# Performance work log

Hardware: AMD Instinct MI355X
Metric: run time of the kernel (lower is better)

The kernel has to match this reference:

```python
import jax, jax.numpy as jnp
import numpy as np

NUM_HEADS = 8
KEY_SIZE = 64
VALUE_SIZE = 64
NUM_GROUPS = 3 * NUM_HEADS  # 24
C = NUM_HEADS * (2 * KEY_SIZE + VALUE_SIZE)  # 1536
EPS = 1e-5


def setup_inputs() -> dict:
    key = jax.random.key(0)
    k1, k2, k3 = jax.random.split(key, 3)
    x = jax.random.normal(k1, (8, C, 32, 32), dtype=jnp.float32)
    # GroupNorm affine params (torch default ones/zeros, perturbed for non-trivial grads)
    gn_weight = 1.0 + 0.1 * jax.random.normal(k2, (C,), dtype=jnp.float32)
    gn_bias = 0.1 * jax.random.normal(k3, (C,), dtype=jnp.float32)
    return {"x": x, "gn_weight": gn_weight, "gn_bias": gn_bias}


def _group_norm(x, weight, bias):
    B, Cc, H, W = x.shape
    xg = x.reshape(B, NUM_GROUPS, -1)  # [B, G, (C/G)*H*W]
    mean = jnp.mean(xg, axis=-1, keepdims=True)
    var = jnp.var(xg, axis=-1, keepdims=True)
    xn = ((xg - mean) * jax.lax.rsqrt(var + EPS)).reshape(B, Cc, H, W)
    return xn * weight[:, None, None] + bias[:, None, None]


def reference(x, gn_weight, gn_bias):
    NH, KS, VS = NUM_HEADS, KEY_SIZE, VALUE_SIZE
    B, Cc, H, W = x.shape
    xn = _group_norm(x, gn_weight, gn_bias)
    xr = xn.reshape(B, NH, 2 * KS + VS, H * W)  # [B, NH, 2KS+VS, NK]
    k = xr[:, :, :KS]            # [B, NH, KS, NK]
    q = xr[:, :, KS:2 * KS]      # [B, NH, KS, NK]
    v = xr[:, :, 2 * KS:]        # [B, NH, VS, NK]
    # saliency = q^T @ k / sqrt(KS) -> [B, NH, NKq, NKk]
    sal = jnp.einsum('bhcq,bhck->bhqk', q, k) / jnp.sqrt(jnp.float32(KS))
    mask = jax.nn.softmax(sal, axis=-1)
    # out = v @ mask^T -> [B, NH, VS, NKq]
    out = jnp.einsum('bhvk,bhqk->bhvq', v, mask)
    return out.reshape(B, NH * VS, H, W)
```

## Files before the change

### kernel.cpp

```cpp
#include <hip/hip_runtime.h>
#include <hip/hip_bf16.h>


typedef __attribute__((ext_vector_type(8))) short bf16x8;
typedef __attribute__((ext_vector_type(4))) float f32x4;
typedef __attribute__((ext_vector_type(16))) float f32x16;
typedef unsigned short u16;
typedef unsigned int u32;

#define SM_SCALE 0.18033688f
#define SM_OFF   8.0f

__device__ __forceinline__ u32 pack2(float a, float b) {
    union { float f; u32 u; } ua, ub; ua.f = a; ub.f = b;
    return __builtin_amdgcn_perm(ub.u + 0x8000u, ua.u + 0x8000u, 0x07060302u);
}
union BB { uint4 u; bf16x8 v; };

__device__ __forceinline__ f32x16 zero16() {
    f32x16 z;
#pragma unroll
    for (int i = 0; i < 16; ++i) z[i] = 0.f;
    return z;
}

__device__ __forceinline__ void swap32(u32 a, u32 b, int hi, u32& ret0, u32& ret1) {
#if __has_builtin(__builtin_amdgcn_permlane32_swap)
    (void)hi;
    auto sw = __builtin_amdgcn_permlane32_swap(a, b, false, false);
    ret0 = sw[0]; ret1 = sw[1];
#else
    u32 pa = __shfl_xor(a, 32), pb = __shfl_xor(b, 32);
    ret0 = hi ? pb : a;
    ret1 = hi ? b : pa;
#endif
}

__global__ __launch_bounds__(256) void gn_partial(const float* __restrict__ x,
                                                  float* __restrict__ partials) {
    int blk = blockIdx.x;
    const float4* p = (const float4*)(x + (size_t)blk * 8192);
    int t = threadIdx.x;
    float s1a = 0.f, s2a = 0.f, s1b = 0.f, s2b = 0.f;
#pragma unroll
    for (int i = 0; i < 8; i += 2) {
        float4 va = p[t + i * 256];
        float4 vb = p[t + (i + 1) * 256];
        s1a += va.x + va.y + va.z + va.w;
        s2a += va.x*va.x + va.y*va.y + va.z*va.z + va.w*va.w;
        s1b += vb.x + vb.y + vb.z + vb.w;
        s2b += vb.x*vb.x + vb.y*vb.y + vb.z*vb.z + vb.w*vb.w;
    }
    float s1 = s1a + s1b, s2 = s2a + s2b;
    for (int off = 32; off > 0; off >>= 1) {
        s1 += __shfl_down(s1, off);
        s2 += __shfl_down(s2, off);
    }
    __shared__ float a1[4], a2[4];
    int wave = t >> 6, lane = t & 63;
    if (lane == 0) { a1[wave] = s1; a2[wave] = s2; }
    __syncthreads();
    if (t == 0) {
        partials[blk * 2 + 0] = a1[0] + a1[1] + a1[2] + a1[3];
        partials[blk * 2 + 1] = a2[0] + a2[1] + a2[2] + a2[3];
    }
}

__device__ __forceinline__ void group_stats(const float* __restrict__ partials,
                                            int bg, float& mean, float& rstd) {
    float s1 = 0.f, s2 = 0.f;
#pragma unroll
    for (int j = 0; j < 8; ++j) {
        s1 += partials[(bg * 8 + j) * 2 + 0];
        s2 += partials[(bg * 8 + j) * 2 + 1];
    }
    mean = s1 * (1.f / 65536.f);
    float var = s2 * (1.f / 65536.f) - mean * mean;
    rstd = rsqrtf(var + 1e-5f);
}

__global__ __launch_bounds__(256, 2) void attn_fused(
    const float* __restrict__ x, const float* __restrict__ gamma,
    const float* __restrict__ beta, const float* __restrict__ partials,
    float* __restrict__ out)
{
    const int bid = blockIdx.x;
    const int qt = bid >> 6;
    const int pair = bid & 63;
    const int b = pair >> 3, h = pair & 7;
    const float* xb = x + (size_t)b * 1536 * 1024;
    const int tid = threadIdx.x;
    const int w = tid >> 6;
    const int lane = tid & 63;
    const int li = lane & 31;
    const int hi = lane >> 5;

    float ms[3], rs[3];
    group_stats(partials, b * 24 + 3 * h + 0, ms[0], rs[0]);
    group_stats(partials, b * 24 + 3 * h + 1, ms[1], rs[1]);
    group_stats(partials, b * 24 + 3 * h + 2, ms[2], rs[2]);

    __shared__ uint4 KT[2][512];
    __shared__ uint4 VT[2][512];

    const int sr = tid & 63;
    const int cc0 = tid >> 6;
    float kw[16], kb[16];
#pragma unroll
    for (int u = 0; u < 16; ++u) {
        int c = ((u < 8) ? cc0 : (cc0 + 4)) * 8 + (u & 7);
        int cg = h * 192 + c;
        kw[u] = gamma[cg] * rs[0];
        kb[u] = beta[cg] - ms[0] * kw[u];
    }
    const int vcg = h * 192 + 128 + sr;
    const float vw = gamma[vcg] * rs[2];
    const float vb = beta[vcg] - ms[2] * vw;

    const int kx = sr & 7;
    const int kidx0 = sr * 8 + (cc0 ^ kx);
    const int kidx1 = sr * 8 + ((cc0 + 4) ^ kx);
    const int vidx0 = sr * 8 + ((cc0 * 2) ^ kx);
    const int vidx1 = sr * 8 + ((cc0 * 2 + 1) ^ kx);

    const float* kbase = xb + (size_t)(h * 192) * 1024 + sr;
    const float* vbase = xb + (size_t)vcg * 1024 + cc0 * 16;

    const int q0 = qt * 128 + w * 32;
    bf16x8 bq[4];
#pragma unroll
    for (int cs = 0; cs < 4; ++cs) {
        u32 qq[4];
#pragma unroll
        for (int jp = 0; jp < 4; ++jp) {
            int cg = h * 192 + 64 + cs * 16 + hi * 8 + jp * 2;
            float w0 = gamma[cg] * rs[1],     b0 = beta[cg] - ms[1] * w0;
            float w1 = gamma[cg + 1] * rs[1], b1 = beta[cg + 1] - ms[1] * w1;
            float a0 = xb[(size_t)cg * 1024 + q0 + li];
            float a1 = xb[(size_t)(cg + 1) * 1024 + q0 + li];
            qq[jp] = pack2(__builtin_fmaf(a0, w0, b0), __builtin_fmaf(a1, w1, b1));
        }
        BB tb; tb.u = uint4{qq[0], qq[1], qq[2], qq[3]};
        bq[cs] = tb.v;
    }

    f32x16 oacc[2];
    oacc[0] = zero16(); oacc[1] = zero16();
    float lsum = 0.f;

    const int x7 = li & 7;

    float rk[16], rv[16];
#define LOAD_TILE(KT_)                                                        \
    {                                                                         \
        const float* kp = kbase + (KT_) * 64;                                 \
        _Pragma("unroll")                                                     \
        for (int u = 0; u < 16; ++u) {                                        \
            int c = ((u < 8) ? cc0 : (cc0 + 4)) * 8 + (u & 7);                \
            rk[u] = kp[(size_t)c * 1024];                                     \
        }                                                                     \
        const float* vp = vbase + (KT_) * 64;                                 \
        _Pragma("unroll")                                                     \
        for (int f = 0; f < 4; ++f) {                                         \
            float4 vq = *(const float4*)(vp + f * 4);                         \
            rv[f * 4 + 0] = vq.x; rv[f * 4 + 1] = vq.y;                       \
            rv[f * 4 + 2] = vq.z; rv[f * 4 + 3] = vq.w;                       \
        }                                                                     \
    }
#define COMMIT_TILE(BUF_)                                                     \
    {                                                                         \
        uint4 ka, kc, va, vc;                                                 \
        ka.x = pack2(__builtin_fmaf(rk[0], kw[0], kb[0]),                     \
                     __builtin_fmaf(rk[1], kw[1], kb[1]));                    \
        ka.y = pack2(__builtin_fmaf(rk[2], kw[2], kb[2]),                     \
                     __builtin_fmaf(rk[3], kw[3], kb[3]));                    \
        ka.z = pack2(__builtin_fmaf(rk[4], kw[4], kb[4]),                     \
                     __builtin_fmaf(rk[5], kw[5], kb[5]));                    \
        ka.w = pack2(__builtin_fmaf(rk[6], kw[6], kb[6]),                     \
                     __builtin_fmaf(rk[7], kw[7], kb[7]));                    \
        kc.x = pack2(__builtin_fmaf(rk[8], kw[8], kb[8]),                     \
                     __builtin_fmaf(rk[9], kw[9], kb[9]));                    \
        kc.y = pack2(__builtin_fmaf(rk[10], kw[10], kb[10]),                  \
                     __builtin_fmaf(rk[11], kw[11], kb[11]));                 \
        kc.z = pack2(__builtin_fmaf(rk[12], kw[12], kb[12]),                  \
                     __builtin_fmaf(rk[13], kw[13], kb[13]));                 \
        kc.w = pack2(__builtin_fmaf(rk[14], kw[14], kb[14]),                  \
                     __builtin_fmaf(rk[15], kw[15], kb[15]));                 \
        va.x = pack2(__builtin_fmaf(rv[0], vw, vb),                           \
                     __builtin_fmaf(rv[1], vw, vb));                          \
        va.y = pack2(__builtin_fmaf(rv[2], vw, vb),                           \
                     __builtin_fmaf(rv[3], vw, vb));                          \
        va.z = pack2(__builtin_fmaf(rv[4], vw, vb),                           \
                     __builtin_fmaf(rv[5], vw, vb));                          \
        va.w = pack2(__builtin_fmaf(rv[6], vw, vb),                           \
                     __builtin_fmaf(rv[7], vw, vb));                          \
        vc.x = pack2(__builtin_fmaf(rv[8], vw, vb),                           \
                     __builtin_fmaf(rv[9], vw, vb));                          \
        vc.y = pack2(__builtin_fmaf(rv[10], vw, vb),                          \
                     __builtin_fmaf(rv[11], vw, vb));                         \
        vc.z = pack2(__builtin_fmaf(rv[12], vw, vb),                          \
                     __builtin_fmaf(rv[13], vw, vb));                         \
        vc.w = pack2(__builtin_fmaf(rv[14], vw, vb),                          \
                     __builtin_fmaf(rv[15], vw, vb));                         \
        KT[BUF_][kidx0] = ka; KT[BUF_][kidx1] = kc;                           \
        VT[BUF_][vidx0] = va; VT[BUF_][vidx1] = vc;                           \
    }

    LOAD_TILE(0);
    COMMIT_TILE(0);
    __syncthreads();

#pragma unroll 2
    for (int kt = 0; kt < 16; ++kt) {
        const int cur = kt & 1;
        if (kt < 15) LOAD_TILE(kt + 1);

        f32x16 sf[2];
#pragma unroll
        for (int kf = 0; kf < 2; ++kf) {
            bf16x8 ak[4];
#pragma unroll
            for (int cs = 0; cs < 4; ++cs)
                ak[cs] = ((const BB*)&KT[cur][(kf * 32 + li) * 8 + ((cs * 2 + hi) ^ x7)])->v;
            f32x16 acc = zero16();
            __builtin_amdgcn_s_setprio(1);
#pragma unroll
            for (int cs = 0; cs < 4; ++cs)
                acc = __builtin_amdgcn_mfma_f32_32x32x16_bf16(ak[cs], bq[cs], acc, 0, 0, 0);
            __builtin_amdgcn_s_setprio(0);
            sf[kf] = acc;
        }

        BB pbv[4];
#pragma unroll
        for (int kf = 0; kf < 2; ++kf)
#pragma unroll
            for (int s = 0; s < 2; ++s) {
                float p0 = exp2f(__builtin_fmaf(sf[kf][8 * s + 0], SM_SCALE, -SM_OFF));
                float p1 = exp2f(__builtin_fmaf(sf[kf][8 * s + 1], SM_SCALE, -SM_OFF));
                float p2 = exp2f(__builtin_fmaf(sf[kf][8 * s + 2], SM_SCALE, -SM_OFF));
                float p3 = exp2f(__builtin_fmaf(sf[kf][8 * s + 3], SM_SCALE, -SM_OFF));
                float p4 = exp2f(__builtin_fmaf(sf[kf][8 * s + 4], SM_SCALE, -SM_OFF));
                float p5 = exp2f(__builtin_fmaf(sf[kf][8 * s + 5], SM_SCALE, -SM_OFF));
                float p6 = exp2f(__builtin_fmaf(sf[kf][8 * s + 6], SM_SCALE, -SM_OFF));
                float p7 = exp2f(__builtin_fmaf(sf[kf][8 * s + 7], SM_SCALE, -SM_OFF));
                lsum += ((p0 + p1) + (p2 + p3)) + ((p4 + p5) + (p6 + p7));
                u32 Pa = pack2(p0, p1), Pb = pack2(p2, p3);
                u32 Pc = pack2(p4, p5), Pd = pack2(p6, p7);
                u32 w0, w1, w2, w3;
                swap32(Pa, Pc, hi, w0, w2);
                swap32(Pb, Pd, hi, w1, w3);
                pbv[kf * 2 + s].u = uint4{w0, w1, w2, w3};
            }

#pragma unroll
        for (int vf = 0; vf < 2; ++vf) {
            bf16x8 av[4];
#pragma unroll
            for (int ks = 0; ks < 4; ++ks)
                av[ks] = ((const BB*)&VT[cur][(vf * 32 + li) * 8 + ((ks * 2 + hi) ^ x7)])->v;
            __builtin_amdgcn_s_setprio(1);
#pragma unroll
            for (int ks = 0; ks < 4; ++ks)
                oacc[vf] = __builtin_amdgcn_mfma_f32_32x32x16_bf16(av[ks], pbv[ks].v, oacc[vf], 0, 0, 0);
            __builtin_amdgcn_s_setprio(0);
        }

        if (kt < 15) COMMIT_TILE(cur ^ 1);
        __syncthreads();
    }

    lsum += __shfl_xor(lsum, 32);
    float invl = 1.f / lsum;
    float* ob = out + (size_t)pair * 65536 + q0 + li;
#pragma unroll
    for (int vf = 0; vf < 2; ++vf)
#pragma unroll
        for (int r = 0; r < 16; ++r) {
            int v = vf * 32 + (r & 3) + 8 * (r >> 2) + 4 * hi;
            ob[(size_t)v * 1024] = oacc[vf][r] * invl;
        }
}

extern "C" void kernel_launch(void* const* d_in, const int* in_sizes, int n_in,
                              void* d_out, int out_size, void* d_ws, size_t ws_size,
                              hipStream_t stream) {
    const float* x     = (const float*)d_in[0];
    const float* gamma = (const float*)d_in[1];
    const float* beta  = (const float*)d_in[2];
    float* out = (float*)d_out;

    float* partials = (float*)d_ws;

    gn_partial<<<1536, 256, 0, stream>>>(x, partials);
    attn_fused<<<512, 256, 0, stream>>>(x, gamma, beta, partials, out);
}
```

Measured before the change: 129.6 us.

## Split key sequence across two warp groups per block with LDS reduction

Doubles the block to 512 threads. Two 256-thread groups each process half of the key tiles (8 of 16) for the same query tile, each with its own double-buffered LDS tiles. Partial output accumulators and row sums are then combined through shared memory before the final normalised store. The goal is to halve the serial key loop per block and raise wave-level parallelism per CU. The cost is higher register and LDS pressure under the tighter launch bounds, duplicated Q loading, and an extra reduction step. The score MFMA and exp stages are also interleaved per key fragment, which cuts the live score registers.

```diff
diff --git a/kernel.cpp b/kernel.cpp
--- a/kernel.cpp
+++ b/kernel.cpp
@@ -79,7 +79,7 @@
     rstd = rsqrtf(var + 1e-5f);
 }
 
-__global__ __launch_bounds__(256, 2) void attn_fused(
+__global__ __launch_bounds__(512, 4) void attn_fused(
     const float* __restrict__ x, const float* __restrict__ gamma,
     const float* __restrict__ beta, const float* __restrict__ partials,
     float* __restrict__ out)
@@ -90,8 +90,10 @@
     const int b = pair >> 3, h = pair & 7;
     const float* xb = x + (size_t)b * 1536 * 1024;
     const int tid = threadIdx.x;
-    const int w = tid >> 6;
-    const int lane = tid & 63;
+    const int wg = tid >> 8;
+    const int t = tid & 255;
+    const int w2 = t >> 6;
+    const int lane = t & 63;
     const int li = lane & 31;
     const int hi = lane >> 5;
 
@@ -100,11 +102,10 @@
     group_stats(partials, b * 24 + 3 * h + 1, ms[1], rs[1]);
     group_stats(partials, b * 24 + 3 * h + 2, ms[2], rs[2]);
 
-    __shared__ uint4 KT[2][512];
-    __shared__ uint4 VT[2][512];
-
-    const int sr = tid & 63;
-    const int cc0 = tid >> 6;
+    __shared__ uint4 TILES[2][2][2][512];
+
+    const int sr = t & 63;
+    const int cc0 = t >> 6;
     float kw[16], kb[16];
 #pragma unroll
     for (int u = 0; u < 16; ++u) {
@@ -126,7 +127,7 @@
     const float* kbase = xb + (size_t)(h * 192) * 1024 + sr;
     const float* vbase = xb + (size_t)vcg * 1024 + cc0 * 16;
 
-    const int q0 = qt * 128 + w * 32;
+    const int q0 = qt * 128 + w2 * 32;
     bf16x8 bq[4];
 #pragma unroll
     for (int cs = 0; cs < 4; ++cs) {
@@ -151,15 +152,15 @@
     const int x7 = li & 7;
 
     float rk[16], rv[16];
-#define LOAD_TILE(KT_)                                                        \
+#define LOAD_TILE(KTG_)                                                       \
     {                                                                         \
-        const float* kp = kbase + (KT_) * 64;                                 \
+        const float* kp = kbase + (KTG_) * 64;                                \
         _Pragma("unroll")                                                     \
         for (int u = 0; u < 16; ++u) {                                        \
             int c = ((u < 8) ? cc0 : (cc0 + 4)) * 8 + (u & 7);                \
             rk[u] = kp[(size_t)c * 1024];                                     \
         }                                                                     \
-        const float* vp = vbase + (KT_) * 64;                                 \
+        const float* vp = vbase + (KTG_) * 64;                                \
         _Pragma("unroll")                                                     \
         for (int f = 0; f < 4; ++f) {                                         \
             float4 vq = *(const float4*)(vp + f * 4);                         \
@@ -202,63 +203,58 @@
                      __builtin_fmaf(rv[13], vw, vb));                         \
         vc.w = pack2(__builtin_fmaf(rv[14], vw, vb),                          \
                      __builtin_fmaf(rv[15], vw, vb));                         \
-        KT[BUF_][kidx0] = ka; KT[BUF_][kidx1] = kc;                           \
-        VT[BUF_][vidx0] = va; VT[BUF_][vidx1] = vc;                           \
-    }
-
-    LOAD_TILE(0);
+        TILES[wg][BUF_][0][kidx0] = ka; TILES[wg][BUF_][0][kidx1] = kc;       \
+        TILES[wg][BUF_][1][vidx0] = va; TILES[wg][BUF_][1][vidx1] = vc;       \
+    }
+
+    LOAD_TILE(wg * 8);
     COMMIT_TILE(0);
     __syncthreads();
 
 #pragma unroll 2
-    for (int kt = 0; kt < 16; ++kt) {
-        const int cur = kt & 1;
-        if (kt < 15) LOAD_TILE(kt + 1);
-
-        f32x16 sf[2];
+    for (int kt8 = 0; kt8 < 8; ++kt8) {
+        const int cur = kt8 & 1;
+        if (kt8 < 7) LOAD_TILE(wg * 8 + kt8 + 1);
+
+        BB pbv[4];
 #pragma unroll
         for (int kf = 0; kf < 2; ++kf) {
             bf16x8 ak[4];
 #pragma unroll
             for (int cs = 0; cs < 4; ++cs)
-                ak[cs] = ((const BB*)&KT[cur][(kf * 32 + li) * 8 + ((cs * 2 + hi) ^ x7)])->v;
+                ak[cs] = ((const BB*)&TILES[wg][cur][0][(kf * 32 + li) * 8 + ((cs * 2 + hi) ^ x7)])->v;
             f32x16 acc = zero16();
             __builtin_amdgcn_s_setprio(1);
 #pragma unroll
             for (int cs = 0; cs < 4; ++cs)
                 acc = __builtin_amdgcn_mfma_f32_32x32x16_bf16(ak[cs], bq[cs], acc, 0, 0, 0);
             __builtin_amdgcn_s_setprio(0);
-            sf[kf] = acc;
-        }
-
-        BB pbv[4];
-#pragma unroll
-        for (int kf = 0; kf < 2; ++kf)
 #pragma unroll
             for (int s = 0; s < 2; ++s) {
-                float p0 = exp2f(__builtin_fmaf(sf[kf][8 * s + 0], SM_SCALE, -SM_OFF));
-                float p1 = exp2f(__builtin_fmaf(sf[kf][8 * s + 1], SM_SCALE, -SM_OFF));
-                float p2 = exp2f(__builtin_fmaf(sf[kf][8 * s + 2], SM_SCALE, -SM_OFF));
-                float p3 = exp2f(__builtin_fmaf(sf[kf][8 * s + 3], SM_SCALE, -SM_OFF));
-                float p4 = exp2f(__builtin_fmaf(sf[kf][8 * s + 4], SM_SCALE, -SM_OFF));
-                float p5 = exp2f(__builtin_fmaf(sf[kf][8 * s + 5], SM_SCALE, -SM_OFF));
-                float p6 = exp2f(__builtin_fmaf(sf[kf][8 * s + 6], SM_SCALE, -SM_OFF));
-                float p7 = exp2f(__builtin_fmaf(sf[kf][8 * s + 7], SM_SCALE, -SM_OFF));
+                float p0 = exp2f(__builtin_fmaf(acc[8 * s + 0], SM_SCALE, -SM_OFF));
+                float p1 = exp2f(__builtin_fmaf(acc[8 * s + 1], SM_SCALE, -SM_OFF));
+                float p2 = exp2f(__builtin_fmaf(acc[8 * s + 2], SM_SCALE, -SM_OFF));
+                float p3 = exp2f(__builtin_fmaf(acc[8 * s + 3], SM_SCALE, -SM_OFF));
+                float p4 = exp2f(__builtin_fmaf(acc[8 * s + 4], SM_SCALE, -SM_OFF));
+                float p5 = exp2f(__builtin_fmaf(acc[8 * s + 5], SM_SCALE, -SM_OFF));
+                float p6 = exp2f(__builtin_fmaf(acc[8 * s + 6], SM_SCALE, -SM_OFF));
+                float p7 = exp2f(__builtin_fmaf(acc[8 * s + 7], SM_SCALE, -SM_OFF));
                 lsum += ((p0 + p1) + (p2 + p3)) + ((p4 + p5) + (p6 + p7));
                 u32 Pa = pack2(p0, p1), Pb = pack2(p2, p3);
                 u32 Pc = pack2(p4, p5), Pd = pack2(p6, p7);
-                u32 w0, w1, w2, w3;
-                swap32(Pa, Pc, hi, w0, w2);
+                u32 w0, w1, w2m, w3;
+                swap32(Pa, Pc, hi, w0, w2m);
                 swap32(Pb, Pd, hi, w1, w3);
-                pbv[kf * 2 + s].u = uint4{w0, w1, w2, w3};
+                pbv[kf * 2 + s].u = uint4{w0, w1, w2m, w3};
             }
+        }
 
 #pragma unroll
         for (int vf = 0; vf < 2; ++vf) {
             bf16x8 av[4];
 #pragma unroll
             for (int ks = 0; ks < 4; ++ks)
-                av[ks] = ((const BB*)&VT[cur][(vf * 32 + li) * 8 + ((ks * 2 + hi) ^ x7)])->v;
+                av[ks] = ((const BB*)&TILES[wg][cur][1][(vf * 32 + li) * 8 + ((ks * 2 + hi) ^ x7)])->v;
             __builtin_amdgcn_s_setprio(1);
 #pragma unroll
             for (int ks = 0; ks < 4; ++ks)
@@ -266,20 +262,33 @@
             __builtin_amdgcn_s_setprio(0);
         }
 
-        if (kt < 15) COMMIT_TILE(cur ^ 1);
+        if (kt8 < 7) COMMIT_TILE(cur ^ 1);
         __syncthreads();
     }
 
     lsum += __shfl_xor(lsum, 32);
-    float invl = 1.f / lsum;
-    float* ob = out + (size_t)pair * 65536 + q0 + li;
-#pragma unroll
-    for (int vf = 0; vf < 2; ++vf)
-#pragma unroll
-        for (int r = 0; r < 16; ++r) {
-            int v = vf * 32 + (r & 3) + 8 * (r >> 2) + 4 * hi;
-            ob[(size_t)v * 1024] = oacc[vf][r] * invl;
-        }
+    float* Osh = (float*)TILES;
+    float* lsh = Osh + 256 * 33;
+    if (wg == 1) {
+#pragma unroll
+        for (int vf = 0; vf < 2; ++vf)
+#pragma unroll
+            for (int r = 0; r < 16; ++r)
+                Osh[t * 33 + vf * 16 + r] = oacc[vf][r];
+        lsh[t] = lsum;
+    }
+    __syncthreads();
+    if (wg == 0) {
+        float invl = 1.f / (lsum + lsh[t]);
+        float* ob = out + (size_t)pair * 65536 + q0 + li;
+#pragma unroll
+        for (int vf = 0; vf < 2; ++vf)
+#pragma unroll
+            for (int r = 0; r < 16; ++r) {
+                int v = vf * 32 + (r & 3) + 8 * (r >> 2) + 4 * hi;
+                ob[(size_t)v * 1024] = (oacc[vf][r] + Osh[t * 33 + vf * 16 + r]) * invl;
+            }
+    }
 }
 
 extern "C" void kernel_launch(void* const* d_in, const int* in_sizes, int n_in,
@@ -293,5 +302,5 @@
     float* partials = (float*)d_ws;
 
     gn_partial<<<1536, 256, 0, stream>>>(x, partials);
-    attn_fused<<<512, 256, 0, stream>>>(x, gamma, beta, partials, out);
-}
+    attn_fused<<<512, 512, 0, stream>>>(x, gamma, beta, partials, out);
+}
```

New measurement: 328.8 us. +153.6%, slower.

## Fold GroupNorm affine of K and V out of the attention inner loop

Applied to the files above, without the earlier changes.

The K normalization scale is folded into the Q fragment, and its bias becomes a per-query constant added to the softmax exponent offset. The V affine is applied once at output time, since the softmax weights sum to one. This lets the per-tile commit pack raw x values to bf16 with no FMAs. The change also switches exp2f to the hardware v_exp intrinsic and interleaves the exponentials with each score MFMA block. The cost is bf16 rounding of un-normalized K and V, and a changed order of the normalization arithmetic.

```diff
diff --git a/kernel.cpp b/kernel.cpp
--- a/kernel.cpp
+++ b/kernel.cpp
@@ -16,6 +16,14 @@
     return __builtin_amdgcn_perm(ub.u + 0x8000u, ua.u + 0x8000u, 0x07060302u);
 }
 union BB { uint4 u; bf16x8 v; };
+
+__device__ __forceinline__ float fexp2(float x) {
+#if __has_builtin(__builtin_amdgcn_exp2f)
+    return __builtin_amdgcn_exp2f(x);
+#else
+    float r; asm("v_exp_f32 %0, %1" : "=v"(r) : "v"(x)); return r;
+#endif
+}
 
 __device__ __forceinline__ f32x16 zero16() {
     f32x16 z;
@@ -90,7 +98,7 @@
     const int b = pair >> 3, h = pair & 7;
     const float* xb = x + (size_t)b * 1536 * 1024;
     const int tid = threadIdx.x;
-    const int w = tid >> 6;
+    const int w2 = tid >> 6;
     const int lane = tid & 63;
     const int li = lane & 31;
     const int hi = lane >> 5;
@@ -105,18 +113,6 @@
 
     const int sr = tid & 63;
     const int cc0 = tid >> 6;
-    float kw[16], kb[16];
-#pragma unroll
-    for (int u = 0; u < 16; ++u) {
-        int c = ((u < 8) ? cc0 : (cc0 + 4)) * 8 + (u & 7);
-        int cg = h * 192 + c;
-        kw[u] = gamma[cg] * rs[0];
-        kb[u] = beta[cg] - ms[0] * kw[u];
-    }
-    const int vcg = h * 192 + 128 + sr;
-    const float vw = gamma[vcg] * rs[2];
-    const float vb = beta[vcg] - ms[2] * vw;
-
     const int kx = sr & 7;
     const int kidx0 = sr * 8 + (cc0 ^ kx);
     const int kidx1 = sr * 8 + ((cc0 + 4) ^ kx);
@@ -124,25 +120,36 @@
     const int vidx1 = sr * 8 + ((cc0 * 2 + 1) ^ kx);
 
     const float* kbase = xb + (size_t)(h * 192) * 1024 + sr;
-    const float* vbase = xb + (size_t)vcg * 1024 + cc0 * 16;
-
-    const int q0 = qt * 128 + w * 32;
+    const float* vbase = xb + (size_t)(h * 192 + 128 + sr) * 1024 + cc0 * 16;
+
+    const int q0 = qt * 128 + w2 * 32;
     bf16x8 bq[4];
+    float dqp = 0.f;
 #pragma unroll
     for (int cs = 0; cs < 4; ++cs) {
         u32 qq[4];
 #pragma unroll
         for (int jp = 0; jp < 4; ++jp) {
-            int cg = h * 192 + 64 + cs * 16 + hi * 8 + jp * 2;
-            float w0 = gamma[cg] * rs[1],     b0 = beta[cg] - ms[1] * w0;
-            float w1 = gamma[cg + 1] * rs[1], b1 = beta[cg + 1] - ms[1] * w1;
-            float a0 = xb[(size_t)cg * 1024 + q0 + li];
-            float a1 = xb[(size_t)(cg + 1) * 1024 + q0 + li];
-            qq[jp] = pack2(__builtin_fmaf(a0, w0, b0), __builtin_fmaf(a1, w1, b1));
+            int c0 = cs * 16 + hi * 8 + jp * 2;
+            int cgq = h * 192 + 64 + c0;
+            int cgk = h * 192 + c0;
+            float wq0 = gamma[cgq] * rs[1],     bq0 = beta[cgq] - ms[1] * wq0;
+            float wq1 = gamma[cgq + 1] * rs[1], bq1 = beta[cgq + 1] - ms[1] * wq1;
+            float wk0 = gamma[cgk] * rs[0],     bk0 = beta[cgk] - ms[0] * wk0;
+            float wk1 = gamma[cgk + 1] * rs[0], bk1 = beta[cgk + 1] - ms[0] * wk1;
+            float a0 = xb[(size_t)cgq * 1024 + q0 + li];
+            float a1 = xb[(size_t)(cgq + 1) * 1024 + q0 + li];
+            float qn0 = __builtin_fmaf(a0, wq0, bq0);
+            float qn1 = __builtin_fmaf(a1, wq1, bq1);
+            dqp = __builtin_fmaf(bk0, qn0, dqp);
+            dqp = __builtin_fmaf(bk1, qn1, dqp);
+            qq[jp] = pack2(qn0 * wk0, qn1 * wk1);
         }
         BB tb; tb.u = uint4{qq[0], qq[1], qq[2], qq[3]};
         bq[cs] = tb.v;
     }
+    const float dq = dqp + __shfl_xor(dqp, 32);
+    const float offq = __builtin_fmaf(dq, SM_SCALE, -SM_OFF);
 
     f32x16 oacc[2];
     oacc[0] = zero16(); oacc[1] = zero16();
@@ -170,38 +177,14 @@
 #define COMMIT_TILE(BUF_)                                                     \
     {                                                                         \
         uint4 ka, kc, va, vc;                                                 \
-        ka.x = pack2(__builtin_fmaf(rk[0], kw[0], kb[0]),                     \
-                     __builtin_fmaf(rk[1], kw[1], kb[1]));                    \
-        ka.y = pack2(__builtin_fmaf(rk[2], kw[2], kb[2]),                     \
-                     __builtin_fmaf(rk[3], kw[3], kb[3]));                    \
-        ka.z = pack2(__builtin_fmaf(rk[4], kw[4], kb[4]),                     \
-                     __builtin_fmaf(rk[5], kw[5], kb[5]));                    \
-        ka.w = pack2(__builtin_fmaf(rk[6], kw[6], kb[6]),                     \
-                     __builtin_fmaf(rk[7], kw[7], kb[7]));                    \
-        kc.x = pack2(__builtin_fmaf(rk[8], kw[8], kb[8]),                     \
-                     __builtin_fmaf(rk[9], kw[9], kb[9]));                    \
-        kc.y = pack2(__builtin_fmaf(rk[10], kw[10], kb[10]),                  \
-                     __builtin_fmaf(rk[11], kw[11], kb[11]));                 \
-        kc.z = pack2(__builtin_fmaf(rk[12], kw[12], kb[12]),                  \
-                     __builtin_fmaf(rk[13], kw[13], kb[13]));                 \
-        kc.w = pack2(__builtin_fmaf(rk[14], kw[14], kb[14]),                  \
-                     __builtin_fmaf(rk[15], kw[15], kb[15]));                 \
-        va.x = pack2(__builtin_fmaf(rv[0], vw, vb),                           \
-                     __builtin_fmaf(rv[1], vw, vb));                          \
-        va.y = pack2(__builtin_fmaf(rv[2], vw, vb),                           \
-                     __builtin_fmaf(rv[3], vw, vb));                          \
-        va.z = pack2(__builtin_fmaf(rv[4], vw, vb),                           \
-                     __builtin_fmaf(rv[5], vw, vb));                          \
-        va.w = pack2(__builtin_fmaf(rv[6], vw, vb),                           \
-                     __builtin_fmaf(rv[7], vw, vb));                          \
-        vc.x = pack2(__builtin_fmaf(rv[8], vw, vb),                           \
-                     __builtin_fmaf(rv[9], vw, vb));                          \
-        vc.y = pack2(__builtin_fmaf(rv[10], vw, vb),                          \
-                     __builtin_fmaf(rv[11], vw, vb));                         \
-        vc.z = pack2(__builtin_fmaf(rv[12], vw, vb),                          \
-                     __builtin_fmaf(rv[13], vw, vb));                         \
-        vc.w = pack2(__builtin_fmaf(rv[14], vw, vb),                          \
-                     __builtin_fmaf(rv[15], vw, vb));                         \
+        ka.x = pack2(rk[0], rk[1]);   ka.y = pack2(rk[2], rk[3]);             \
+        ka.z = pack2(rk[4], rk[5]);   ka.w = pack2(rk[6], rk[7]);             \
+        kc.x = pack2(rk[8], rk[9]);   kc.y = pack2(rk[10], rk[11]);           \
+        kc.z = pack2(rk[12], rk[13]); kc.w = pack2(rk[14], rk[15]);           \
+        va.x = pack2(rv[0], rv[1]);   va.y = pack2(rv[2], rv[3]);             \
+        va.z = pack2(rv[4], rv[5]);   va.w = pack2(rv[6], rv[7]);             \
+        vc.x = pack2(rv[8], rv[9]);   vc.y = pack2(rv[10], rv[11]);           \
+        vc.z = pack2(rv[12], rv[13]); vc.w = pack2(rv[14], rv[15]);           \
         KT[BUF_][kidx0] = ka; KT[BUF_][kidx1] = kc;                           \
         VT[BUF_][vidx0] = va; VT[BUF_][vidx1] = vc;                           \
     }
@@ -215,7 +198,7 @@
         const int cur = kt & 1;
         if (kt < 15) LOAD_TILE(kt + 1);
 
-        f32x16 sf[2];
+        BB pbv[4];
 #pragma unroll
         for (int kf = 0; kf < 2; ++kf) {
             bf16x8 ak[4];
@@ -228,30 +211,25 @@
             for (int cs = 0; cs < 4; ++cs)
                 acc = __builtin_amdgcn_mfma_f32_32x32x16_bf16(ak[cs], bq[cs], acc, 0, 0, 0);
             __builtin_amdgcn_s_setprio(0);
-            sf[kf] = acc;
-        }
-
-        BB pbv[4];
-#pragma unroll
-        for (int kf = 0; kf < 2; ++kf)
 #pragma unroll
             for (int s = 0; s < 2; ++s) {
-                float p0 = exp2f(__builtin_fmaf(sf[kf][8 * s + 0], SM_SCALE, -SM_OFF));
-                float p1 = exp2f(__builtin_fmaf(sf[kf][8 * s + 1], SM_SCALE, -SM_OFF));
-                float p2 = exp2f(__builtin_fmaf(sf[kf][8 * s + 2], SM_SCALE, -SM_OFF));
-                float p3 = exp2f(__builtin_fmaf(sf[kf][8 * s + 3], SM_SCALE, -SM_OFF));
-                float p4 = exp2f(__builtin_fmaf(sf[kf][8 * s + 4], SM_SCALE, -SM_OFF));
-                float p5 = exp2f(__builtin_fmaf(sf[kf][8 * s + 5], SM_SCALE, -SM_OFF));
-                float p6 = exp2f(__builtin_fmaf(sf[kf][8 * s + 6], SM_SCALE, -SM_OFF));
-                float p7 = exp2f(__builtin_fmaf(sf[kf][8 * s + 7], SM_SCALE, -SM_OFF));
+                float p0 = fexp2(__builtin_fmaf(acc[8 * s + 0], SM_SCALE, offq));
+                float p1 = fexp2(__builtin_fmaf(acc[8 * s + 1], SM_SCALE, offq));
+                float p2 = fexp2(__builtin_fmaf(acc[8 * s + 2], SM_SCALE, offq));
+                float p3 = fexp2(__builtin_fmaf(acc[8 * s + 3], SM_SCALE, offq));
+                float p4 = fexp2(__builtin_fmaf(acc[8 * s + 4], SM_SCALE, offq));
+                float p5 = fexp2(__builtin_fmaf(acc[8 * s + 5], SM_SCALE, offq));
+                float p6 = fexp2(__builtin_fmaf(acc[8 * s + 6], SM_SCALE, offq));
+                float p7 = fexp2(__builtin_fmaf(acc[8 * s + 7], SM_SCALE, offq));
                 lsum += ((p0 + p1) + (p2 + p3)) + ((p4 + p5) + (p6 + p7));
                 u32 Pa = pack2(p0, p1), Pb = pack2(p2, p3);
                 u32 Pc = pack2(p4, p5), Pd = pack2(p6, p7);
-                u32 w0, w1, w2, w3;
-                swap32(Pa, Pc, hi, w0, w2);
+                u32 w0, w1, w2m, w3;
+                swap32(Pa, Pc, hi, w0, w2m);
                 swap32(Pb, Pd, hi, w1, w3);
-                pbv[kf * 2 + s].u = uint4{w0, w1, w2, w3};
+                pbv[kf * 2 + s].u = uint4{w0, w1, w2m, w3};
             }
+        }
 
 #pragma unroll
         for (int vf = 0; vf < 2; ++vf) {
@@ -278,7 +256,10 @@
 #pragma unroll
         for (int r = 0; r < 16; ++r) {
             int v = vf * 32 + (r & 3) + 8 * (r >> 2) + 4 * hi;
-            ob[(size_t)v * 1024] = oacc[vf][r] * invl;
+            int cgv = h * 192 + 128 + v;
+            float wv = gamma[cgv] * rs[2];
+            float bvv = beta[cgv] - ms[2] * wv;
+            ob[(size_t)v * 1024] = __builtin_fmaf(oacc[vf][r] * invl, wv, bvv);
         }
 }
 
```

Result: faster. 121.0 us (-6.7%).
